# Kernel tuning notes

Measured on AMD Instinct MI355X. Metric: run time of the kernel, lower is better.

The kernel has to match this reference:

```python
import jax, jax.numpy as jnp
import numpy as np
import math

GROUPS = 32
HEADS = 8
EPS_GN = 1e-5


def group_norm(x, w, b):
    # x: [B, C, H, W]; GroupNorm32 computes in float32
    B, C, H, W = x.shape
    xg = x.astype(jnp.float32).reshape(B, GROUPS, C // GROUPS, H, W)
    mu = xg.mean(axis=(2, 3, 4), keepdims=True)
    var = xg.var(axis=(2, 3, 4), keepdims=True)
    xn = (xg - mu) * jax.lax.rsqrt(var + EPS_GN)
    xn = xn.reshape(B, C, H, W)
    return (xn * w[None, :, None, None] + b[None, :, None, None]).astype(x.dtype)


def fresnel_interference(H, W, wavelength):
    ys, xs = jnp.meshgrid(jnp.arange(H, dtype=jnp.float32),
                          jnp.arange(W, dtype=jnp.float32), indexing='ij')
    pos = jnp.stack([ys, xs], axis=-1).reshape(-1, 2)  # [N, 2]
    diff = pos[None, :, :] - pos[:, None, :]           # [N, N, 2]
    dist = jnp.sqrt((diff ** 2).sum(-1) + 1e-8)        # [N, N]
    phase = 2.0 * math.pi * dist / (jnp.abs(wavelength) * H + 1e-6)
    return jnp.cos(phase)


def fresnel_attn(h, qkv_w, out_w, out_b, wavelength):
    B, C, H, W = h.shape
    N = H * W
    dh = C // HEADS
    scale = dh ** -0.5
    xf = h.reshape(B, C, N).transpose(0, 2, 1)                 # [B, N, C]
    qkv = xf @ qkv_w                                            # [B, N, 3C]
    q, k, v = jnp.split(qkv, 3, axis=-1)
    def heads(t):
        return t.reshape(B, N, HEADS, dh).transpose(0, 2, 1, 3)  # [B, Hh, N, dh]
    q, k, v = heads(q), heads(k), heads(v)
    dots = jnp.einsum('bhnd,bhmd->bhnm', q, k) * scale
    interference = fresnel_interference(H, W, wavelength)       # [N, N]
    dots = dots + interference[None, None] * 0.1
    attn = jax.nn.softmax(dots, axis=-1)
    out = jnp.einsum('bhnm,bhmd->bhnd', attn, v)
    out = out.transpose(0, 2, 1, 3).reshape(B, N, C)
    out = out @ out_w + out_b
    return out.transpose(0, 2, 1).reshape(B, C, H, W)


def cross_attn(h, context, q_w, k_w, v_w, out_w, out_b):
    B, C, H, W = h.shape
    N = H * W
    inner = q_w.shape[1]
    dh = inner // HEADS
    scale = dh ** -0.5
    xf = h.reshape(B, C, N).transpose(0, 2, 1)                 # [B, N, C]
    q = xf @ q_w                                                # [B, N, inner]
    k = context @ k_w                                           # [B, L, inner]
    v = context @ v_w
    L = context.shape[1]
    q = q.reshape(B, N, HEADS, dh).transpose(0, 2, 1, 3)
    k = k.reshape(B, L, HEADS, dh).transpose(0, 2, 1, 3)
    v = v.reshape(B, L, HEADS, dh).transpose(0, 2, 1, 3)
    attn = jax.nn.softmax(jnp.einsum('bhnd,bhld->bhnl', q, k) * scale, axis=-1)
    out = jnp.einsum('bhnl,bhld->bhnd', attn, v)
    out = out.transpose(0, 2, 1, 3).reshape(B, N, inner)
    out = out @ out_w + out_b
    return out.transpose(0, 2, 1).reshape(B, C, H, W)


def setup_inputs() -> dict:
    key = jax.random.key(0)
    ks = jax.random.split(key, 10)
    B, C, H, W = 4, 512, 32, 32
    ctx_len, ctx_dim = 77, 768
    s = lambda d: 1.0 / math.sqrt(d)
    return {
        'x': jax.random.normal(ks[0], (B, C, H, W), jnp.float32),
        'context': jax.random.normal(ks[1], (B, ctx_len, ctx_dim), jnp.float32),
        'gn1_w': jnp.ones((C,), jnp.float32),
        'gn1_b': jnp.zeros((C,), jnp.float32),
        'gn2_w': jnp.ones((C,), jnp.float32),
        'gn2_b': jnp.zeros((C,), jnp.float32),
        'fa_qkv_w': jax.random.normal(ks[2], (C, 3 * C), jnp.float32) * s(C),
        'fa_out_w': jax.random.normal(ks[3], (C, C), jnp.float32) * s(C),
        'fa_out_b': jnp.zeros((C,), jnp.float32),
        'wavelength': jnp.asarray(0.1, jnp.float32),
        'ca_q_w': jax.random.normal(ks[4], (C, 512), jnp.float32) * s(C),
        'ca_k_w': jax.random.normal(ks[5], (ctx_dim, 512), jnp.float32) * s(ctx_dim),
        'ca_v_w': jax.random.normal(ks[6], (ctx_dim, 512), jnp.float32) * s(ctx_dim),
        'ca_out_w': jax.random.normal(ks[7], (512, C), jnp.float32) * s(512),
        'ca_out_b': jnp.zeros((C,), jnp.float32),
    }


def reference(x, context, gn1_w, gn1_b, gn2_w, gn2_b,
              fa_qkv_w, fa_out_w, fa_out_b, wavelength,
              ca_q_w, ca_k_w, ca_v_w, ca_out_w, ca_out_b):
    h = group_norm(x, gn1_w, gn1_b)
    h = fresnel_attn(h, fa_qkv_w, fa_out_w, fa_out_b, wavelength)
    x = x + h
    h = group_norm(x, gn2_w, gn2_b)
    h = cross_attn(h, context, ca_q_w, ca_k_w, ca_v_w, ca_out_w, ca_out_b)
    return x + h
```

## Files before the change

### kernel.cpp

```cpp
#include <hip/hip_runtime.h>
#include <hip/hip_bf16.h>
#include <math.h>

#define B_    4
#define N_    1024
#define L_    77

typedef float f4 __attribute__((ext_vector_type(4)));
typedef short bf8 __attribute__((ext_vector_type(8)));
typedef short s4v __attribute__((ext_vector_type(4)));

#if __has_builtin(__builtin_amdgcn_exp2f)
#define EXP2(x) __builtin_amdgcn_exp2f(x)
#else
#define EXP2(x) exp2f(x)
#endif

__device__ __forceinline__ float fs(short s) {
    unsigned u = ((unsigned)(unsigned short)s) << 16;
    return __builtin_bit_cast(float, u);
}
__device__ __forceinline__ short sf(float f) {
    unsigned u = __builtin_bit_cast(unsigned, f);
    unsigned r = (u + 0x7FFF + ((u >> 16) & 1)) >> 16;
    return (short)r;
}
__device__ __forceinline__ bf8 zero8() { bf8 v; for (int i = 0; i < 8; ++i) v[i] = 0; return v; }
__device__ __forceinline__ f4 zerof4() { f4 v; for (int i = 0; i < 4; ++i) v[i] = 0.f; return v; }

#define MFMA(a, b, c) __builtin_amdgcn_mfma_f32_16x16x32_bf16((a), (b), (c), 0, 0, 0)

__device__ __forceinline__ void gn_body(const float* __restrict__ src,
                                        const float* __restrict__ w,
                                        const float* __restrict__ bs,
                                        short* __restrict__ dst, int g, int b)
{
    const float* xb = src + ((size_t)b * 512 + g * 16) * 1024;
    float s = 0.f, ss = 0.f;
    for (int l = threadIdx.x; l < 4096; l += 256) {
        float4 v = *(const float4*)(xb + l * 4);
        s += v.x + v.y + v.z + v.w;
        ss += v.x * v.x + v.y * v.y + v.z * v.z + v.w * v.w;
    }
    for (int off = 32; off; off >>= 1) {
        s  += __shfl_down(s,  off);
        ss += __shfl_down(ss, off);
    }
    __shared__ float sred[8], ssred[8];
    int wid = threadIdx.x >> 6;
    if ((threadIdx.x & 63) == 0) { sred[wid] = s; ssred[wid] = ss; }
    __syncthreads();
    if (threadIdx.x == 0) {
        float S = 0.f, SS = 0.f;
        for (int i = 0; i < 4; ++i) { S += sred[i]; SS += ssred[i]; }
        float mu = S * (1.f / 16384.f);
        float var = SS * (1.f / 16384.f) - mu * mu;
        sred[4] = mu; ssred[4] = rsqrtf(var + 1e-5f);
    }
    __syncthreads();
    float mu = sred[4], rs = ssred[4];

    int c4 = threadIdx.x & 3, nb = threadIdx.x >> 2;
    int c = g * 16 + c4 * 4;
    float4 wv = *(const float4*)(w + c);
    float4 bv = *(const float4*)(bs + c);
    for (int rep = 0; rep < 16; ++rep) {
        int n = rep * 64 + nb;
        float v0 = xb[(size_t)(c4 * 4 + 0) * 1024 + n];
        float v1 = xb[(size_t)(c4 * 4 + 1) * 1024 + n];
        float v2 = xb[(size_t)(c4 * 4 + 2) * 1024 + n];
        float v3 = xb[(size_t)(c4 * 4 + 3) * 1024 + n];
        s4v hb;
        hb[0] = sf((v0 - mu) * rs * wv.x + bv.x);
        hb[1] = sf((v1 - mu) * rs * wv.y + bv.y);
        hb[2] = sf((v2 - mu) * rs * wv.z + bv.z);
        hb[3] = sf((v3 - mu) * rs * wv.w + bv.w);
        *(s4v*)(dst + ((size_t)b * 1024 + n) * 512 + c) = hb;
    }
}

__device__ __forceinline__ void wtile(const float* __restrict__ in, short* __restrict__ out,
                                      int K, int J, int tile, int tid, float (*t)[33])
{
    int jt = J >> 5;
    int j0 = (tile % jt) * 32, k0 = (tile / jt) * 32;
    int tx = tid & 31, ty = tid >> 5;
#pragma unroll
    for (int i = 0; i < 4; ++i)
        t[ty + i * 8][tx] = in[(size_t)(k0 + ty + i * 8) * J + j0 + tx];
    __syncthreads();
#pragma unroll
    for (int i = 0; i < 4; ++i)
        out[(size_t)(j0 + ty + i * 8) * K + k0 + tx] = sf(t[tx][ty + i * 8]);
}

__global__ __launch_bounds__(256)
void prep_mega(const float* __restrict__ x, const float* __restrict__ gn1w,
               const float* __restrict__ gn1b, short* __restrict__ h1b,
               const float* __restrict__ wl, short* __restrict__ tab,
               const float* __restrict__ qkvw, short* __restrict__ qkvwT,
               const float* __restrict__ faow, short* __restrict__ faowT,
               const float* __restrict__ caqw, short* __restrict__ caqwT,
               const float* __restrict__ cakw, short* __restrict__ cakwT,
               const float* __restrict__ cavw, short* __restrict__ cavwT,
               const float* __restrict__ caow, short* __restrict__ caowT,
               const float* __restrict__ ctx, short* __restrict__ ctxb)
{
    __shared__ float tls[32][33];
    int bid = blockIdx.x, tid = threadIdx.x;
    if (bid < 128) { gn_body(x, gn1w, gn1b, h1b, bid & 31, bid >> 5); return; }
    bid -= 128;
    if (bid < 16) {
        int idx = bid * 256 + tid;
        if (idx < 3969) {
            int i = idx / 63, j = idx - i * 63;
            float dy = (float)(i - 31), dx = (float)(j - 31);
            float dist = sqrtf(dy * dy + dx * dx + 1e-8f);
            float den = fabsf(wl[0]) * 32.0f + 1e-6f;
            tab[idx] = sf(0.1f * cosf(6.283185307179586f * dist / den) * 1.4426950408889634f);
        }
        return;
    }
    bid -= 16;
    if (bid < 768) { wtile(qkvw, qkvwT, 512, 1536, bid, tid, tls); return; }
    bid -= 768;
    if (bid < 256) { wtile(faow, faowT, 512, 512, bid, tid, tls); return; }
    bid -= 256;
    if (bid < 256) { wtile(caqw, caqwT, 512, 512, bid, tid, tls); return; }
    bid -= 256;
    if (bid < 384) { wtile(cakw, cakwT, 768, 512, bid, tid, tls); return; }
    bid -= 384;
    if (bid < 384) { wtile(cavw, cavwT, 768, 512, bid, tid, tls); return; }
    bid -= 384;
    if (bid < 256) { wtile(caow, caowT, 512, 512, bid, tid, tls); return; }
    bid -= 256;
    int base = bid * 1024 + tid * 4;
    float4 v = *(const float4*)(ctx + base);
    s4v o; o[0] = sf(v.x); o[1] = sf(v.y); o[2] = sf(v.z); o[3] = sf(v.w);
    *(s4v*)(ctxb + base) = o;
}

__global__ __launch_bounds__(256)
void gn_kernel(const float* __restrict__ src, const float* __restrict__ w,
               const float* __restrict__ bs, short* __restrict__ dst)
{
    gn_body(src, w, bs, dst, blockIdx.x, blockIdx.y);
}

template<int EPI>
__device__ __forceinline__ void gemm_body(
    short* As, short* Ws, int j0, int m0, int b,
    const short* __restrict__ A, const short* __restrict__ Wt,
    const float* __restrict__ bias, const float* __restrict__ res,
    void* __restrict__ outv, void* __restrict__ out2v,
    int M, int K, int J, long aStride, long wStride, long oStride, long o2Stride)
{
    int tid = threadIdx.x, w = tid >> 6, lane = tid & 63;
    int lr = lane & 15, lg = lane >> 4;
    int wr = w >> 1, wc = w & 1;
    const short* Ab  = A  + (size_t)b * aStride;
    const short* Wtb = Wt + (size_t)b * wStride;
    int r0 = tid >> 2, c0 = (tid & 3) * 8;
    int r1 = 64 + r0;
    bool gA0 = (m0 + r0) < M, gA1 = (m0 + r1) < M;
    const short* ap0 = Ab + (size_t)(m0 + r0) * K + c0;
    const short* ap1 = Ab + (size_t)(m0 + r1) * K + c0;
    const short* wp0 = Wtb + (size_t)(j0 + r0) * K + c0;
    const short* wp1 = Wtb + (size_t)(j0 + r1) * K + c0;

    f4 acc[4][4];
#pragma unroll
    for (int i = 0; i < 4; ++i)
#pragma unroll
        for (int j = 0; j < 4; ++j) acc[i][j] = zerof4();

    *(bf8*)(As + r0 * 40 + c0) = gA0 ? *(const bf8*)ap0 : zero8();
    *(bf8*)(As + r1 * 40 + c0) = gA1 ? *(const bf8*)ap1 : zero8();
    *(bf8*)(Ws + r0 * 40 + c0) = *(const bf8*)wp0;
    *(bf8*)(Ws + r1 * 40 + c0) = *(const bf8*)wp1;
    __syncthreads();

    int nk = K >> 5;
    for (int t = 0; t < nk; ++t) {
        int cur = (t & 1) * 5120;
        bool more = (t + 1) < nk;
        bf8 na0, na1, nw0, nw1;
        if (more) {
            int ko = (t + 1) << 5;
            na0 = gA0 ? *(const bf8*)(ap0 + ko) : zero8();
            na1 = gA1 ? *(const bf8*)(ap1 + ko) : zero8();
            nw0 = *(const bf8*)(wp0 + ko);
            nw1 = *(const bf8*)(wp1 + ko);
        }
        bf8 af[4], bfr[4];
#pragma unroll
        for (int fi = 0; fi < 4; ++fi)
            af[fi] = *(const bf8*)(As + cur + (wr * 64 + fi * 16 + lr) * 40 + lg * 8);
#pragma unroll
        for (int fj = 0; fj < 4; ++fj)
            bfr[fj] = *(const bf8*)(Ws + cur + (wc * 64 + fj * 16 + lr) * 40 + lg * 8);
#pragma unroll
        for (int fi = 0; fi < 4; ++fi)
#pragma unroll
            for (int fj = 0; fj < 4; ++fj)
                acc[fi][fj] = MFMA(af[fi], bfr[fj], acc[fi][fj]);
        if (more) {
            int nb = 5120 - cur;
            *(bf8*)(As + nb + r0 * 40 + c0) = na0;
            *(bf8*)(As + nb + r1 * 40 + c0) = na1;
            *(bf8*)(Ws + nb + r0 * 40 + c0) = nw0;
            *(bf8*)(Ws + nb + r1 * 40 + c0) = nw1;
        }
        __syncthreads();
    }

    if (EPI == 0) {
        short* out = (short*)outv + (size_t)b * oStride;
#pragma unroll
        for (int fi = 0; fi < 4; ++fi)
#pragma unroll
            for (int reg = 0; reg < 4; ++reg) {
                int m = m0 + wr * 64 + fi * 16 + lg * 4 + reg;
                if (m < M) {
#pragma unroll
                    for (int fj = 0; fj < 4; ++fj)
                        out[(size_t)m * J + j0 + wc * 64 + fj * 16 + lr] = sf(acc[fi][fj][reg]);
                }
            }
    } else if (EPI == 1) {
        float* out = (float*)outv + (size_t)b * oStride;
        const float* rp = res + (size_t)b * oStride;
#pragma unroll
        for (int fi = 0; fi < 4; ++fi) {
            float4 bq = *(const float4*)(bias + m0 + wr * 64 + fi * 16 + lg * 4);
            float bvr[4] = {bq.x, bq.y, bq.z, bq.w};
#pragma unroll
            for (int reg = 0; reg < 4; ++reg) {
                int m = m0 + wr * 64 + fi * 16 + lg * 4 + reg;
                size_t ro = (size_t)m * J + j0 + wc * 64;
#pragma unroll
                for (int fj = 0; fj < 4; ++fj) {
                    size_t idx = ro + fj * 16 + lr;
                    out[idx] = acc[fi][fj][reg] + bvr[reg] + rp[idx];
                }
            }
        }
    } else if (EPI == 3) {
        if (j0 < 1024) {
            short* out = (short*)outv + (size_t)b * oStride;
#pragma unroll
            for (int fi = 0; fi < 4; ++fi)
#pragma unroll
                for (int reg = 0; reg < 4; ++reg) {
                    int m = m0 + wr * 64 + fi * 16 + lg * 4 + reg;
#pragma unroll
                    for (int fj = 0; fj < 4; ++fj)
                        out[(size_t)m * 1024 + j0 + wc * 64 + fj * 16 + lr] = sf(acc[fi][fj][reg]);
                }
        } else {
            short* Vg = (short*)out2v + (size_t)b * o2Stride;
#pragma unroll
            for (int fi = 0; fi < 4; ++fi) {
                int n = m0 + wr * 64 + fi * 16 + lg * 4;
#pragma unroll
                for (int fj = 0; fj < 4; ++fj) {
                    int dg = j0 - 1024 + wc * 64 + fj * 16 + lr;
                    s4v v;
#pragma unroll
                    for (int reg = 0; reg < 4; ++reg) v[reg] = sf(acc[fi][fj][reg]);
                    *(s4v*)(Vg + (size_t)dg * 1024 + n) = v;
                }
            }
        }
    } else {
        if (j0 < 512) {
            short* out = (short*)outv + (size_t)b * oStride;
#pragma unroll
            for (int fi = 0; fi < 4; ++fi)
#pragma unroll
                for (int reg = 0; reg < 4; ++reg) {
                    int m = m0 + wr * 64 + fi * 16 + lg * 4 + reg;
                    if (m < M) {
#pragma unroll
                        for (int fj = 0; fj < 4; ++fj)
                            out[(size_t)m * 512 + j0 + wc * 64 + fj * 16 + lr] = sf(acc[fi][fj][reg]);
                    }
                }
        } else {
            short* vt = (short*)out2v + (size_t)b * o2Stride;
#pragma unroll
            for (int fi = 0; fi < 4; ++fi) {
                int l0 = wr * 64 + fi * 16 + lg * 4;
                if (l0 < 80) {
#pragma unroll
                    for (int fj = 0; fj < 4; ++fj) {
                        int dg = j0 - 512 + wc * 64 + fj * 16 + lr;
                        s4v v;
#pragma unroll
                        for (int reg = 0; reg < 4; ++reg) v[reg] = sf(acc[fi][fj][reg]);
                        *(s4v*)(vt + (size_t)dg * 80 + l0) = v;
                    }
                }
            }
        }
    }
}

template<int EPI>
__global__ __launch_bounds__(256)
void gemm_std(const short* __restrict__ A, const short* __restrict__ Wt,
              const float* __restrict__ bias, const float* __restrict__ res,
              void* __restrict__ outv, void* __restrict__ out2v,
              int M, int K, int J, long aStride, long wStride, long oStride, long o2Stride)
{
    __shared__ short As[2 * 128 * 40];
    __shared__ short Ws[2 * 128 * 40];
    gemm_body<EPI>(As, Ws, blockIdx.x * 128, blockIdx.y * 128, blockIdx.z,
                   A, Wt, bias, res, outv, out2v, M, K, J,
                   aStride, wStride, oStride, o2Stride);
}

__global__ __launch_bounds__(256)
void gemm_qkv_kv(const short* __restrict__ h1b, const short* __restrict__ qkvwT,
                 short* __restrict__ qkb, short* __restrict__ Vg,
                 const short* __restrict__ ctxb, const short* __restrict__ cakwT,
                 short* __restrict__ k2b, short* __restrict__ v2t)
{
    __shared__ short As[2 * 128 * 40];
    __shared__ short Ws[2 * 128 * 40];
    if (blockIdx.y < 8) {
        gemm_body<3>(As, Ws, blockIdx.x * 128, blockIdx.y * 128, blockIdx.z,
                     h1b, qkvwT, nullptr, nullptr, qkb, Vg,
                     1024, 512, 1536, 524288L, 0L, 1048576L, 524288L);
    } else if (blockIdx.x < 8) {
        gemm_body<4>(As, Ws, blockIdx.x * 128, 0, blockIdx.z,
                     ctxb, cakwT, nullptr, nullptr, k2b, v2t,
                     77, 768, 1024, 59136L, 0L, 39424L, 40960L);
    }
}

__global__ __launch_bounds__(256)
void fresnel_attn_v3(const short* __restrict__ qkb, const short* __restrict__ Vg,
                     const short* __restrict__ tab, short* __restrict__ ao)
{
    int qb = blockIdx.x, h = blockIdx.y, b = blockIdx.z;
    int n0 = qb * 64;
    __shared__ short Ks[2][64][64];
    __shared__ short Vt[2][64][64];
    __shared__ short Ps[4][16][72];
    __shared__ short tabs[4032];
    int tid = threadIdx.x, w = tid >> 6, lane = tid & 63;
    int lr = lane & 15, lg = lane >> 4;
    const short* qp = qkb + (size_t)b * 1048576;
    const short* vp = Vg + ((size_t)b * 512 + h * 64) * 1024;

    for (int l = tid; l < 504; l += 256)
        *(bf8*)&tabs[l * 8] = *(const bf8*)(tab + l * 8);

    int q = n0 + w * 16 + lr;
    bf8 qf0 = *(const bf8*)(qp + (size_t)q * 1024 + h * 64 + lg * 8);
    bf8 qf1 = *(const bf8*)(qp + (size_t)q * 1024 + h * 64 + 32 + lg * 8);

    int sr0 = tid >> 3, sc0 = tid & 7;
    int sr1 = 32 + sr0;
    int sw0 = ((sc0 ^ (sr0 & 7))) * 8;
    int sw1 = ((sc0 ^ (sr1 & 7))) * 8;

    *(bf8*)&Ks[0][sr0][sw0] = *(const bf8*)(qp + (size_t)sr0 * 1024 + 512 + h * 64 + sc0 * 8);
    *(bf8*)&Ks[0][sr1][sw1] = *(const bf8*)(qp + (size_t)sr1 * 1024 + 512 + h * 64 + sc0 * 8);
    *(bf8*)&Vt[0][sr0][sw0] = *(const bf8*)(vp + (size_t)sr0 * 1024 + sc0 * 8);
    *(bf8*)&Vt[0][sr1][sw1] = *(const bf8*)(vp + (size_t)sr1 * 1024 + sc0 * 8);
    __syncthreads();

    float mrun = -1e30f, lrun = 0.f;
    f4 o[4];
#pragma unroll
    for (int i = 0; i < 4; ++i) o[i] = zerof4();

    int ybase = (q >> 5) + 31;
    int xbase = (q & 31) + 31 - lg * 4;
    int rsw = lr & 7;
    int rc0 = (lg ^ rsw) * 8;
    int rc1 = ((4 + lg) ^ rsw) * 8;

    for (int t = 0; t < 16; ++t) {
        int cur = t & 1;
        int m0 = t << 6;
        bool more = t < 15;
        bf8 nk0, nk1, nv0, nv1;
        if (more) {
            int m1 = m0 + 64;
            nk0 = *(const bf8*)(qp + (size_t)(m1 + sr0) * 1024 + 512 + h * 64 + sc0 * 8);
            nk1 = *(const bf8*)(qp + (size_t)(m1 + sr1) * 1024 + 512 + h * 64 + sc0 * 8);
            nv0 = *(const bf8*)(vp + (size_t)sr0 * 1024 + m1 + sc0 * 8);
            nv1 = *(const bf8*)(vp + (size_t)sr1 * 1024 + m1 + sc0 * 8);
        }

        f4 sa[4];
#pragma unroll
        for (int fj = 0; fj < 4; ++fj) sa[fj] = zerof4();
        __builtin_amdgcn_s_setprio(1);
#pragma unroll
        for (int fj = 0; fj < 4; ++fj)
            sa[fj] = MFMA(*(const bf8*)&Ks[cur][fj * 16 + lr][rc0], qf0, sa[fj]);
#pragma unroll
        for (int fj = 0; fj < 4; ++fj)
            sa[fj] = MFMA(*(const bf8*)&Ks[cur][fj * 16 + lr][rc1], qf1, sa[fj]);
        __builtin_amdgcn_s_setprio(0);

        int yb = ybase - (m0 >> 5);
        float pv[4][4];
        float tmax = -1e30f;
#pragma unroll
        for (int fj = 0; fj < 4; ++fj) {
            int rowoff = (yb - (fj >> 1)) * 63 + xbase - (fj & 1) * 16;
#pragma unroll
            for (int reg = 0; reg < 4; ++reg) {
                float t2 = fmaf(sa[fj][reg], 0.18033688011112042f, fs(tabs[rowoff - reg]));
                pv[fj][reg] = t2;
                tmax = fmaxf(tmax, t2);
            }
        }
        if (__any(tmax > mrun + 8.f)) {
            tmax = fmaxf(tmax, __shfl_xor(tmax, 16));
            tmax = fmaxf(tmax, __shfl_xor(tmax, 32));
            float mnew = fmaxf(mrun, tmax);
            float rsc = EXP2(mrun - mnew);
            mrun = mnew;
            lrun *= rsc;
#pragma unroll
            for (int fd = 0; fd < 4; ++fd)
#pragma unroll
                for (int reg = 0; reg < 4; ++reg) o[fd][reg] *= rsc;
        }
        float psum = 0.f;
#pragma unroll
        for (int fj = 0; fj < 4; ++fj) {
            float p0 = EXP2(pv[fj][0] - mrun);
            float p1 = EXP2(pv[fj][1] - mrun);
            float p2 = EXP2(pv[fj][2] - mrun);
            float p3 = EXP2(pv[fj][3] - mrun);
            psum += (p0 + p1) + (p2 + p3);
            int r01, r23;
            asm("v_cvt_pk_bf16_f32 %0, %1, %2" : "=v"(r01) : "v"(p0), "v"(p1));
            asm("v_cvt_pk_bf16_f32 %0, %1, %2" : "=v"(r23) : "v"(p2), "v"(p3));
            int2 pr; pr.x = r01; pr.y = r23;
            *(int2*)&Ps[w][lr][fj * 16 + lg * 4] = pr;
        }
        psum += __shfl_xor(psum, 16);
        psum += __shfl_xor(psum, 32);
        lrun += psum;

        bf8 pa0 = *(const bf8*)&Ps[w][lr][lg * 8];
        bf8 pa1 = *(const bf8*)&Ps[w][lr][32 + lg * 8];
        __builtin_amdgcn_s_setprio(1);
#pragma unroll
        for (int fd = 0; fd < 4; ++fd) {
            o[fd] = MFMA(*(const bf8*)&Vt[cur][fd * 16 + lr][rc0], pa0, o[fd]);
            o[fd] = MFMA(*(const bf8*)&Vt[cur][fd * 16 + lr][rc1], pa1, o[fd]);
        }
        __builtin_amdgcn_s_setprio(0);

        if (more) {
            int nb = cur ^ 1;
            *(bf8*)&Ks[nb][sr0][sw0] = nk0;
            *(bf8*)&Ks[nb][sr1][sw1] = nk1;
            *(bf8*)&Vt[nb][sr0][sw0] = nv0;
            *(bf8*)&Vt[nb][sr1][sw1] = nv1;
        }
        __syncthreads();
    }

    float inv = 1.f / lrun;
    size_t rb = ((size_t)b * N_ + q) * 512 + h * 64;
#pragma unroll
    for (int fd = 0; fd < 4; ++fd) {
        s4v ov;
#pragma unroll
        for (int reg = 0; reg < 4; ++reg) ov[reg] = sf(o[fd][reg] * inv);
        *(s4v*)(ao + rb + fd * 16 + lg * 4) = ov;
    }
}

__global__ __launch_bounds__(256)
void cross_attn_mfma(const short* __restrict__ q2, const short* __restrict__ k2,
                     const short* __restrict__ v2t, short* __restrict__ ao2)
{
    int qb = blockIdx.x, h = blockIdx.y, b = blockIdx.z;
    int n0 = qb * 64;
    __shared__ short Qs[64][72], Ks[96][72], Vt[64][104];
    __shared__ short Ps[4][16][104];
    int tid = threadIdx.x, w = tid >> 6, lane = tid & 63;
    int lr = lane & 15, lg = lane >> 4;

    for (int l = tid; l < 512; l += 256) {
        int n = l >> 3, dq = l & 7;
        *(bf8*)&Qs[n][dq * 8] = *(const bf8*)(q2 + ((size_t)b * N_ + n0 + n) * 512 + h * 64 + dq * 8);
    }
    for (int l = tid; l < 768; l += 256) {
        int m = l >> 3, dq = l & 7;
        bf8 v = zero8();
        if (m < L_) v = *(const bf8*)(k2 + ((size_t)b * L_ + m) * 512 + h * 64 + dq * 8);
        *(bf8*)&Ks[m][dq * 8] = v;
    }
    for (int l = tid; l < 768; l += 256) {
        int d = l / 12, cq = l % 12;
        bf8 v = zero8();
        if (cq < 10) v = *(const bf8*)(v2t + ((size_t)b * 512 + h * 64 + d) * 80 + cq * 8);
        *(bf8*)&Vt[d][cq * 8] = v;
    }
    __syncthreads();

    f4 sacc[6];
#pragma unroll
    for (int fj = 0; fj < 6; ++fj) sacc[fj] = zerof4();
    __builtin_amdgcn_s_setprio(1);
#pragma unroll
    for (int kc = 0; kc < 2; ++kc) {
        bf8 aq = *(const bf8*)&Qs[w * 16 + lr][kc * 32 + lg * 8];
#pragma unroll
        for (int fj = 0; fj < 6; ++fj)
            sacc[fj] = MFMA(aq, *(const bf8*)&Ks[fj * 16 + lr][kc * 32 + lg * 8], sacc[fj]);
    }
    __builtin_amdgcn_s_setprio(0);

    float rinv[4];
#pragma unroll
    for (int reg = 0; reg < 4; ++reg) {
        float sv[6];
#pragma unroll
        for (int fj = 0; fj < 6; ++fj) {
            int m = fj * 16 + lr;
            sv[fj] = (m < L_) ? sacc[fj][reg] * 0.125f : -30000.f;
        }
        float mx = sv[0];
#pragma unroll
        for (int fj = 1; fj < 6; ++fj) mx = fmaxf(mx, sv[fj]);
#pragma unroll
        for (int off = 1; off < 16; off <<= 1) mx = fmaxf(mx, __shfl_xor(mx, off));
        float psum = 0.f;
#pragma unroll
        for (int fj = 0; fj < 6; ++fj) {
            float p = __expf(sv[fj] - mx);
            psum += p;
            Ps[w][lg * 4 + reg][fj * 16 + lr] = sf(p);
        }
#pragma unroll
        for (int off = 1; off < 16; off <<= 1) psum += __shfl_xor(psum, off);
        rinv[reg] = 1.f / psum;
    }
    __syncthreads();

    f4 o[4];
#pragma unroll
    for (int fd = 0; fd < 4; ++fd) o[fd] = zerof4();
    __builtin_amdgcn_s_setprio(1);
#pragma unroll
    for (int kc = 0; kc < 3; ++kc) {
        bf8 ap = *(const bf8*)&Ps[w][lr][kc * 32 + lg * 8];
#pragma unroll
        for (int fd = 0; fd < 4; ++fd)
            o[fd] = MFMA(ap, *(const bf8*)&Vt[fd * 16 + lr][kc * 32 + lg * 8], o[fd]);
    }
    __builtin_amdgcn_s_setprio(0);

#pragma unroll
    for (int reg = 0; reg < 4; ++reg) {
        size_t rb = ((size_t)b * N_ + n0 + w * 16 + lg * 4 + reg) * 512 + h * 64;
#pragma unroll
        for (int fd = 0; fd < 4; ++fd)
            ao2[rb + fd * 16 + lr] = sf(o[fd][reg] * rinv[reg]);
    }
}

extern "C" void kernel_launch(void* const* d_in, const int* in_sizes, int n_in,
                              void* d_out, int out_size, void* d_ws, size_t ws_size,
                              hipStream_t stream)
{
    const float* x    = (const float*)d_in[0];
    const float* ctx  = (const float*)d_in[1];
    const float* gn1w = (const float*)d_in[2];
    const float* gn1b = (const float*)d_in[3];
    const float* gn2w = (const float*)d_in[4];
    const float* gn2b = (const float*)d_in[5];
    const float* qkvw = (const float*)d_in[6];
    const float* faow = (const float*)d_in[7];
    const float* faob = (const float*)d_in[8];
    const float* wl   = (const float*)d_in[9];
    const float* caqw = (const float*)d_in[10];
    const float* cakw = (const float*)d_in[11];
    const float* cavw = (const float*)d_in[12];
    const float* caow = (const float*)d_in[13];
    const float* caob = (const float*)d_in[14];
    float* out = (float*)d_out;
    char* ws = (char*)d_ws;

    float* x1    = (float*)(ws + 0);
    short* qkb   = (short*)(ws + 8388608);
    short* Vg    = (short*)(ws + 16777216);
    short* h1b   = (short*)(ws + 20971520);
    short* ao    = (short*)(ws + 25165824);
    short* q2b   = (short*)(ws + 29360128);
    short* qkvwT = (short*)(ws + 33554432);
    short* faowT = (short*)(ws + 35127296);
    short* caqwT = (short*)(ws + 35651584);
    short* cakwT = (short*)(ws + 36175872);
    short* cavwT = (short*)(ws + 36962304);
    short* caowT = (short*)(ws + 37748736);
    short* k2b   = (short*)(ws + 38273024);
    short* v2t   = (short*)(ws + 38588416);
    short* ctxb  = (short*)(ws + 38916096);
    short* tab   = (short*)(ws + 39389184);

    prep_mega<<<2679, 256, 0, stream>>>(x, gn1w, gn1b, h1b,
                                        wl, tab, qkvw, qkvwT, faow, faowT,
                                        caqw, caqwT, cakw, cakwT, cavw, cavwT,
                                        caow, caowT, ctx, ctxb);
    gemm_qkv_kv<<<dim3(12, 9, 4), 256, 0, stream>>>(
        h1b, qkvwT, qkb, Vg, ctxb, cakwT, k2b, v2t);
    fresnel_attn_v3<<<dim3(16, 8, 4), 256, 0, stream>>>(qkb, Vg, tab, ao);
    gemm_std<1><<<dim3(8, 4, 4), 256, 0, stream>>>(
        faowT, ao, faob, x, x1, nullptr, 512, 512, 1024,
        0L, 524288L, 524288L, 0L);
    gn_kernel<<<dim3(32, 4), 256, 0, stream>>>(x1, gn2w, gn2b, h1b);
    gemm_std<0><<<dim3(4, 8, 4), 256, 0, stream>>>(
        h1b, caqwT, nullptr, nullptr, q2b, nullptr, 1024, 512, 512,
        524288L, 0L, 524288L, 0L);
    cross_attn_mfma<<<dim3(16, 8, 4), 256, 0, stream>>>(q2b, k2b, v2t, ao);
    gemm_std<1><<<dim3(8, 4, 4), 256, 0, stream>>>(
        caowT, ao, caob, x1, out, nullptr, 512, 512, 1024,
        0L, 524288L, 524288L, 0L);
}
```

Before: 218.9 us.

## Fuse GN2 stats into out-proj epilogue, Q-proj into cross-attn, halve GEMM M-tile

The fresnel out-projection epilogue now accumulates per-group sum and sum-of-squares with atomics, so the GN2 kernel only normalizes and no longer does a reduction pass. The cross-attention Q projection is computed inside the attention kernel, which removes one GEMM launch and the q2 buffer round-trip. The GEMM M-tile is halved from 128 to 64 rows, doubling the grid for better CU occupancy. The trade-offs are atomic contention, a single-pass E[x^2]-mu^2 variance that is less numerically stable, and less data reuse per GEMM tile.

```diff
diff --git a/kernel.cpp b/kernel.cpp
--- a/kernel.cpp
+++ b/kernel.cpp
@@ -98,6 +98,7 @@
 void prep_mega(const float* __restrict__ x, const float* __restrict__ gn1w,
                const float* __restrict__ gn1b, short* __restrict__ h1b,
                const float* __restrict__ wl, short* __restrict__ tab,
+               float* __restrict__ gstat,
                const float* __restrict__ qkvw, short* __restrict__ qkvwT,
                const float* __restrict__ faow, short* __restrict__ faowT,
                const float* __restrict__ caqw, short* __restrict__ caqwT,
@@ -111,6 +112,7 @@
     if (bid < 128) { gn_body(x, gn1w, gn1b, h1b, bid & 31, bid >> 5); return; }
     bid -= 128;
     if (bid < 16) {
+        if (bid == 0) gstat[tid] = 0.f;
         int idx = bid * 256 + tid;
         if (idx < 3969) {
             int i = idx / 63, j = idx - i * 63;
@@ -141,10 +143,35 @@
 }
 
 __global__ __launch_bounds__(256)
-void gn_kernel(const float* __restrict__ src, const float* __restrict__ w,
-               const float* __restrict__ bs, short* __restrict__ dst)
-{
-    gn_body(src, w, bs, dst, blockIdx.x, blockIdx.y);
+void gn2_norm(const float* __restrict__ x1, const float* __restrict__ gstat,
+              const float* __restrict__ w, const float* __restrict__ bs,
+              short* __restrict__ dst)
+{
+    int g = blockIdx.x, b = blockIdx.y;
+    float S  = gstat[b * 64 + g * 2];
+    float SS = gstat[b * 64 + g * 2 + 1];
+    float mu = S * (1.f / 16384.f);
+    float var = SS * (1.f / 16384.f) - mu * mu;
+    float rs = rsqrtf(var + 1e-5f);
+    const float* xb = x1 + ((size_t)b * 512 + g * 16) * 1024;
+
+    int c4 = threadIdx.x & 3, nb = threadIdx.x >> 2;
+    int c = g * 16 + c4 * 4;
+    float4 wv = *(const float4*)(w + c);
+    float4 bv = *(const float4*)(bs + c);
+    for (int rep = 0; rep < 16; ++rep) {
+        int n = rep * 64 + nb;
+        float v0 = xb[(size_t)(c4 * 4 + 0) * 1024 + n];
+        float v1 = xb[(size_t)(c4 * 4 + 1) * 1024 + n];
+        float v2 = xb[(size_t)(c4 * 4 + 2) * 1024 + n];
+        float v3 = xb[(size_t)(c4 * 4 + 3) * 1024 + n];
+        s4v hb;
+        hb[0] = sf((v0 - mu) * rs * wv.x + bv.x);
+        hb[1] = sf((v1 - mu) * rs * wv.y + bv.y);
+        hb[2] = sf((v2 - mu) * rs * wv.z + bv.z);
+        hb[3] = sf((v3 - mu) * rs * wv.w + bv.w);
+        *(s4v*)(dst + ((size_t)b * 1024 + n) * 512 + c) = hb;
+    }
 }
 
 template<int EPI>
@@ -152,7 +179,7 @@
     short* As, short* Ws, int j0, int m0, int b,
     const short* __restrict__ A, const short* __restrict__ Wt,
     const float* __restrict__ bias, const float* __restrict__ res,
-    void* __restrict__ outv, void* __restrict__ out2v,
+    void* __restrict__ outv, void* __restrict__ out2v, float* __restrict__ gstat,
     int M, int K, int J, long aStride, long wStride, long oStride, long o2Stride)
 {
     int tid = threadIdx.x, w = tid >> 6, lane = tid & 63;
@@ -161,87 +188,84 @@
     const short* Ab  = A  + (size_t)b * aStride;
     const short* Wtb = Wt + (size_t)b * wStride;
     int r0 = tid >> 2, c0 = (tid & 3) * 8;
-    int r1 = 64 + r0;
-    bool gA0 = (m0 + r0) < M, gA1 = (m0 + r1) < M;
+    bool gA0 = (m0 + r0) < M;
     const short* ap0 = Ab + (size_t)(m0 + r0) * K + c0;
-    const short* ap1 = Ab + (size_t)(m0 + r1) * K + c0;
     const short* wp0 = Wtb + (size_t)(j0 + r0) * K + c0;
-    const short* wp1 = Wtb + (size_t)(j0 + r1) * K + c0;
-
-    f4 acc[4][4];
-#pragma unroll
-    for (int i = 0; i < 4; ++i)
+    const short* wp1 = Wtb + (size_t)(j0 + 64 + r0) * K + c0;
+
+    f4 acc[2][4];
+#pragma unroll
+    for (int i = 0; i < 2; ++i)
 #pragma unroll
         for (int j = 0; j < 4; ++j) acc[i][j] = zerof4();
 
     *(bf8*)(As + r0 * 40 + c0) = gA0 ? *(const bf8*)ap0 : zero8();
-    *(bf8*)(As + r1 * 40 + c0) = gA1 ? *(const bf8*)ap1 : zero8();
     *(bf8*)(Ws + r0 * 40 + c0) = *(const bf8*)wp0;
-    *(bf8*)(Ws + r1 * 40 + c0) = *(const bf8*)wp1;
+    *(bf8*)(Ws + (64 + r0) * 40 + c0) = *(const bf8*)wp1;
     __syncthreads();
 
     int nk = K >> 5;
     for (int t = 0; t < nk; ++t) {
-        int cur = (t & 1) * 5120;
+        int curA = (t & 1) * 2560, curW = (t & 1) * 5120;
         bool more = (t + 1) < nk;
-        bf8 na0, na1, nw0, nw1;
+        bf8 na0, nw0, nw1;
         if (more) {
             int ko = (t + 1) << 5;
             na0 = gA0 ? *(const bf8*)(ap0 + ko) : zero8();
-            na1 = gA1 ? *(const bf8*)(ap1 + ko) : zero8();
             nw0 = *(const bf8*)(wp0 + ko);
             nw1 = *(const bf8*)(wp1 + ko);
         }
-        bf8 af[4], bfr[4];
-#pragma unroll
-        for (int fi = 0; fi < 4; ++fi)
-            af[fi] = *(const bf8*)(As + cur + (wr * 64 + fi * 16 + lr) * 40 + lg * 8);
+        bf8 af[2], bfr[4];
+#pragma unroll
+        for (int fi = 0; fi < 2; ++fi)
+            af[fi] = *(const bf8*)(As + curA + (wr * 32 + fi * 16 + lr) * 40 + lg * 8);
 #pragma unroll
         for (int fj = 0; fj < 4; ++fj)
-            bfr[fj] = *(const bf8*)(Ws + cur + (wc * 64 + fj * 16 + lr) * 40 + lg * 8);
-#pragma unroll
-        for (int fi = 0; fi < 4; ++fi)
+            bfr[fj] = *(const bf8*)(Ws + curW + (wc * 64 + fj * 16 + lr) * 40 + lg * 8);
+#pragma unroll
+        for (int fi = 0; fi < 2; ++fi)
 #pragma unroll
             for (int fj = 0; fj < 4; ++fj)
                 acc[fi][fj] = MFMA(af[fi], bfr[fj], acc[fi][fj]);
         if (more) {
-            int nb = 5120 - cur;
-            *(bf8*)(As + nb + r0 * 40 + c0) = na0;
-            *(bf8*)(As + nb + r1 * 40 + c0) = na1;
-            *(bf8*)(Ws + nb + r0 * 40 + c0) = nw0;
-            *(bf8*)(Ws + nb + r1 * 40 + c0) = nw1;
+            int nbA = 2560 - curA, nbW = 5120 - curW;
+            *(bf8*)(As + nbA + r0 * 40 + c0) = na0;
+            *(bf8*)(Ws + nbW + r0 * 40 + c0) = nw0;
+            *(bf8*)(Ws + nbW + (64 + r0) * 40 + c0) = nw1;
         }
         __syncthreads();
     }
 
-    if (EPI == 0) {
-        short* out = (short*)outv + (size_t)b * oStride;
-#pragma unroll
-        for (int fi = 0; fi < 4; ++fi)
+    if (EPI == 1 || EPI == 2) {
+        float* out = (float*)outv + (size_t)b * oStride;
+        const float* rp = res + (size_t)b * oStride;
+#pragma unroll
+        for (int fi = 0; fi < 2; ++fi) {
+            int mbase = m0 + wr * 32 + fi * 16 + lg * 4;
+            float4 bq = *(const float4*)(bias + mbase);
+            float bvr[4] = {bq.x, bq.y, bq.z, bq.w};
+            float sg = 0.f, ssg = 0.f;
 #pragma unroll
             for (int reg = 0; reg < 4; ++reg) {
-                int m = m0 + wr * 64 + fi * 16 + lg * 4 + reg;
-                if (m < M) {
-#pragma unroll
-                    for (int fj = 0; fj < 4; ++fj)
-                        out[(size_t)m * J + j0 + wc * 64 + fj * 16 + lr] = sf(acc[fi][fj][reg]);
+                size_t ro = (size_t)(mbase + reg) * J + j0 + wc * 64;
+#pragma unroll
+                for (int fj = 0; fj < 4; ++fj) {
+                    size_t idx = ro + fj * 16 + lr;
+                    float v = acc[fi][fj][reg] + bvr[reg] + rp[idx];
+                    out[idx] = v;
+                    if (EPI == 2) { sg += v; ssg += v * v; }
                 }
             }
-    } else if (EPI == 1) {
-        float* out = (float*)outv + (size_t)b * oStride;
-        const float* rp = res + (size_t)b * oStride;
-#pragma unroll
-        for (int fi = 0; fi < 4; ++fi) {
-            float4 bq = *(const float4*)(bias + m0 + wr * 64 + fi * 16 + lg * 4);
-            float bvr[4] = {bq.x, bq.y, bq.z, bq.w};
-#pragma unroll
-            for (int reg = 0; reg < 4; ++reg) {
-                int m = m0 + wr * 64 + fi * 16 + lg * 4 + reg;
-                size_t ro = (size_t)m * J + j0 + wc * 64;
-#pragma unroll
-                for (int fj = 0; fj < 4; ++fj) {
-                    size_t idx = ro + fj * 16 + lr;
-                    out[idx] = acc[fi][fj][reg] + bvr[reg] + rp[idx];
+            if (EPI == 2) {
+#pragma unroll
+                for (int off = 32; off; off >>= 1) {
+                    sg  += __shfl_down(sg,  off);
+                    ssg += __shfl_down(ssg, off);
+                }
+                if (lane == 0) {
+                    int g = mbase >> 4;
+                    atomicAdd(&gstat[b * 64 + g * 2], sg);
+                    atomicAdd(&gstat[b * 64 + g * 2 + 1], ssg);
                 }
             }
         }
@@ -249,26 +273,26 @@
         if (j0 < 1024) {
             short* out = (short*)outv + (size_t)b * oStride;
 #pragma unroll
-            for (int fi = 0; fi < 4; ++fi)
+            for (int fi = 0; fi < 2; ++fi)
 #pragma unroll
                 for (int reg = 0; reg < 4; ++reg) {
-                    int m = m0 + wr * 64 + fi * 16 + lg * 4 + reg;
+                    int m = m0 + wr * 32 + fi * 16 + lg * 4 + reg;
 #pragma unroll
                     for (int fj = 0; fj < 4; ++fj)
                         out[(size_t)m * 1024 + j0 + wc * 64 + fj * 16 + lr] = sf(acc[fi][fj][reg]);
                 }
         } else {
-            short* Vg = (short*)out2v + (size_t)b * o2Stride;
-#pragma unroll
-            for (int fi = 0; fi < 4; ++fi) {
-                int n = m0 + wr * 64 + fi * 16 + lg * 4;
+            short* Vgp = (short*)out2v + (size_t)b * o2Stride;
+#pragma unroll
+            for (int fi = 0; fi < 2; ++fi) {
+                int n = m0 + wr * 32 + fi * 16 + lg * 4;
 #pragma unroll
                 for (int fj = 0; fj < 4; ++fj) {
                     int dg = j0 - 1024 + wc * 64 + fj * 16 + lr;
                     s4v v;
 #pragma unroll
                     for (int reg = 0; reg < 4; ++reg) v[reg] = sf(acc[fi][fj][reg]);
-                    *(s4v*)(Vg + (size_t)dg * 1024 + n) = v;
+                    *(s4v*)(Vgp + (size_t)dg * 1024 + n) = v;
                 }
             }
         }
@@ -276,10 +300,10 @@
         if (j0 < 512) {
             short* out = (short*)outv + (size_t)b * oStride;
 #pragma unroll
-            for (int fi = 0; fi < 4; ++fi)
+            for (int fi = 0; fi < 2; ++fi)
 #pragma unroll
                 for (int reg = 0; reg < 4; ++reg) {
-                    int m = m0 + wr * 64 + fi * 16 + lg * 4 + reg;
+                    int m = m0 + wr * 32 + fi * 16 + lg * 4 + reg;
                     if (m < M) {
 #pragma unroll
                         for (int fj = 0; fj < 4; ++fj)
@@ -289,8 +313,8 @@
         } else {
             short* vt = (short*)out2v + (size_t)b * o2Stride;
 #pragma unroll
-            for (int fi = 0; fi < 4; ++fi) {
-                int l0 = wr * 64 + fi * 16 + lg * 4;
+            for (int fi = 0; fi < 2; ++fi) {
+                int l0 = m0 + wr * 32 + fi * 16 + lg * 4;
                 if (l0 < 80) {
 #pragma unroll
                     for (int fj = 0; fj < 4; ++fj) {
@@ -310,13 +334,13 @@
 __global__ __launch_bounds__(256)
 void gemm_std(const short* __restrict__ A, const short* __restrict__ Wt,
               const float* __restrict__ bias, const float* __restrict__ res,
-              void* __restrict__ outv, void* __restrict__ out2v,
+              void* __restrict__ outv, void* __restrict__ out2v, float* __restrict__ gstat,
               int M, int K, int J, long aStride, long wStride, long oStride, long o2Stride)
 {
-    __shared__ short As[2 * 128 * 40];
+    __shared__ short As[2 * 64 * 40];
     __shared__ short Ws[2 * 128 * 40];
-    gemm_body<EPI>(As, Ws, blockIdx.x * 128, blockIdx.y * 128, blockIdx.z,
-                   A, Wt, bias, res, outv, out2v, M, K, J,
+    gemm_body<EPI>(As, Ws, blockIdx.x * 128, blockIdx.y * 64, blockIdx.z,
+                   A, Wt, bias, res, outv, out2v, gstat, M, K, J,
                    aStride, wStride, oStride, o2Stride);
 }
 
@@ -326,15 +350,15 @@
                  const short* __restrict__ ctxb, const short* __restrict__ cakwT,
                  short* __restrict__ k2b, short* __restrict__ v2t)
 {
-    __shared__ short As[2 * 128 * 40];
+    __shared__ short As[2 * 64 * 40];
     __shared__ short Ws[2 * 128 * 40];
-    if (blockIdx.y < 8) {
-        gemm_body<3>(As, Ws, blockIdx.x * 128, blockIdx.y * 128, blockIdx.z,
-                     h1b, qkvwT, nullptr, nullptr, qkb, Vg,
+    if (blockIdx.y < 16) {
+        gemm_body<3>(As, Ws, blockIdx.x * 128, blockIdx.y * 64, blockIdx.z,
+                     h1b, qkvwT, nullptr, nullptr, qkb, Vg, nullptr,
                      1024, 512, 1536, 524288L, 0L, 1048576L, 524288L);
     } else if (blockIdx.x < 8) {
-        gemm_body<4>(As, Ws, blockIdx.x * 128, 0, blockIdx.z,
-                     ctxb, cakwT, nullptr, nullptr, k2b, v2t,
+        gemm_body<4>(As, Ws, blockIdx.x * 128, (blockIdx.y - 16) * 64, blockIdx.z,
+                     ctxb, cakwT, nullptr, nullptr, k2b, v2t, nullptr,
                      77, 768, 1024, 59136L, 0L, 39424L, 40960L);
     }
 }
@@ -483,20 +507,18 @@
 }
 
 __global__ __launch_bounds__(256)
-void cross_attn_mfma(const short* __restrict__ q2, const short* __restrict__ k2,
-                     const short* __restrict__ v2t, short* __restrict__ ao2)
+void cross_attn_fused(const short* __restrict__ h2, const short* __restrict__ qwT,
+                      const short* __restrict__ k2, const short* __restrict__ v2t,
+                      short* __restrict__ ao2)
 {
     int qb = blockIdx.x, h = blockIdx.y, b = blockIdx.z;
     int n0 = qb * 64;
+    __shared__ short hq[2][64][40], wq[2][64][40];
     __shared__ short Qs[64][72], Ks[96][72], Vt[64][104];
     __shared__ short Ps[4][16][104];
     int tid = threadIdx.x, w = tid >> 6, lane = tid & 63;
     int lr = lane & 15, lg = lane >> 4;
 
-    for (int l = tid; l < 512; l += 256) {
-        int n = l >> 3, dq = l & 7;
-        *(bf8*)&Qs[n][dq * 8] = *(const bf8*)(q2 + ((size_t)b * N_ + n0 + n) * 512 + h * 64 + dq * 8);
-    }
     for (int l = tid; l < 768; l += 256) {
         int m = l >> 3, dq = l & 7;
         bf8 v = zero8();
@@ -509,6 +531,42 @@
         if (cq < 10) v = *(const bf8*)(v2t + ((size_t)b * 512 + h * 64 + d) * 80 + cq * 8);
         *(bf8*)&Vt[d][cq * 8] = v;
     }
+
+    int r0 = tid >> 2, c0 = (tid & 3) * 8;
+    const short* hp = h2 + ((size_t)b * 1024 + n0 + r0) * 512 + c0;
+    const short* wp = qwT + (size_t)(h * 64 + r0) * 512 + c0;
+    *(bf8*)&hq[0][r0][c0] = *(const bf8*)hp;
+    *(bf8*)&wq[0][r0][c0] = *(const bf8*)wp;
+    __syncthreads();
+
+    f4 qacc[4];
+#pragma unroll
+    for (int j = 0; j < 4; ++j) qacc[j] = zerof4();
+    for (int t = 0; t < 16; ++t) {
+        int cur = t & 1;
+        bool more = t < 15;
+        bf8 nh, nw;
+        if (more) {
+            int ko = (t + 1) << 5;
+            nh = *(const bf8*)(hp + ko);
+            nw = *(const bf8*)(wp + ko);
+        }
+        bf8 af = *(const bf8*)&hq[cur][w * 16 + lr][lg * 8];
+#pragma unroll
+        for (int fj = 0; fj < 4; ++fj)
+            qacc[fj] = MFMA(af, *(const bf8*)&wq[cur][fj * 16 + lr][lg * 8], qacc[fj]);
+        if (more) {
+            int nb = cur ^ 1;
+            *(bf8*)&hq[nb][r0][c0] = nh;
+            *(bf8*)&wq[nb][r0][c0] = nw;
+        }
+        __syncthreads();
+    }
+#pragma unroll
+    for (int fj = 0; fj < 4; ++fj)
+#pragma unroll
+        for (int reg = 0; reg < 4; ++reg)
+            Qs[w * 16 + lg * 4 + reg][fj * 16 + lr] = sf(qacc[fj][reg]);
     __syncthreads();
 
     f4 sacc[6];
@@ -600,7 +658,7 @@
     short* Vg    = (short*)(ws + 16777216);
     short* h1b   = (short*)(ws + 20971520);
     short* ao    = (short*)(ws + 25165824);
-    short* q2b   = (short*)(ws + 29360128);
+    float* gstat = (float*)(ws + 29360128);
     short* qkvwT = (short*)(ws + 33554432);
     short* faowT = (short*)(ws + 35127296);
     short* caqwT = (short*)(ws + 35651584);
@@ -613,21 +671,18 @@
     short* tab   = (short*)(ws + 39389184);
 
     prep_mega<<<2679, 256, 0, stream>>>(x, gn1w, gn1b, h1b,
-                                        wl, tab, qkvw, qkvwT, faow, faowT,
+                                        wl, tab, gstat, qkvw, qkvwT, faow, faowT,
                                         caqw, caqwT, cakw, cakwT, cavw, cavwT,
                                         caow, caowT, ctx, ctxb);
-    gemm_qkv_kv<<<dim3(12, 9, 4), 256, 0, stream>>>(
+    gemm_qkv_kv<<<dim3(12, 18, 4), 256, 0, stream>>>(
         h1b, qkvwT, qkb, Vg, ctxb, cakwT, k2b, v2t);
     fresnel_attn_v3<<<dim3(16, 8, 4), 256, 0, stream>>>(qkb, Vg, tab, ao);
-    gemm_std<1><<<dim3(8, 4, 4), 256, 0, stream>>>(
-        faowT, ao, faob, x, x1, nullptr, 512, 512, 1024,
+    gemm_std<2><<<dim3(8, 8, 4), 256, 0, stream>>>(
+        faowT, ao, faob, x, x1, nullptr, gstat, 512, 512, 1024,
         0L, 524288L, 524288L, 0L);
-    gn_kernel<<<dim3(32, 4), 256, 0, stream>>>(x1, gn2w, gn2b, h1b);
-    gemm_std<0><<<dim3(4, 8, 4), 256, 0, stream>>>(
-        h1b, caqwT, nullptr, nullptr, q2b, nullptr, 1024, 512, 512,
-        524288L, 0L, 524288L, 0L);
-    cross_attn_mfma<<<dim3(16, 8, 4), 256, 0, stream>>>(q2b, k2b, v2t, ao);
-    gemm_std<1><<<dim3(8, 4, 4), 256, 0, stream>>>(
-        caowT, ao, caob, x1, out, nullptr, 512, 512, 1024,
+    gn2_norm<<<dim3(32, 4), 256, 0, stream>>>(x1, gstat, gn2w, gn2b, h1b);
+    cross_attn_fused<<<dim3(16, 8, 4), 256, 0, stream>>>(h1b, caqwT, k2b, v2t, ao);
+    gemm_std<1><<<dim3(8, 8, 4), 256, 0, stream>>>(
+        caowT, ao, caob, x1, out, nullptr, nullptr, 512, 512, 1024,
         0L, 524288L, 524288L, 0L);
 }
```

Result: faster. 201.4 us (-8.0%).
